# Performance work log

Hardware: AMD Instinct MI355X
Metric: run time of the kernel (lower is better)

## Reference

```python
import jax, jax.numpy as jnp
import numpy as np

N_NODES = 100000
N_EDGES = 1000000
DIM = 64


def rel_graph_conv(x, src, dst, etype, W, Ws, b, act):
    # DGL RelGraphConv (regularizer=None, self_loop=True, bias=True, sum agg):
    # out_i = act( sum_{(j->i)} W_{r} x_j + x_i @ Ws + b )
    # num_rels=2: transform once per relation, then select per edge.
    h = jnp.einsum('nd,rdo->rno', x, W)              # [2, N, out]
    m = jnp.where((etype == 0)[:, None], h[0][src], h[1][src])  # [E, out]
    agg = jax.ops.segment_sum(m, dst, num_segments=x.shape[0])  # [N, out]
    out = agg + x @ Ws + b
    return act(out) if act is not None else out


def setup_inputs() -> dict:
    key = jax.random.key(0)
    ks = jax.random.split(key, 16)
    scale = 1.0 / np.sqrt(DIM)
    inp = {
        'features': jax.random.normal(ks[0], (N_NODES, DIM), dtype=jnp.float32),
        'src': jax.random.randint(ks[1], (N_EDGES,), 0, N_NODES, dtype=jnp.int32),
        'dst': jax.random.randint(ks[2], (N_EDGES,), 0, N_NODES, dtype=jnp.int32),
        'etype': jax.random.randint(ks[3], (N_EDGES,), 0, 2, dtype=jnp.int32),
    }
    for i in range(3):
        inp[f'W{i}'] = jax.random.normal(ks[4 + 3 * i], (2, DIM, DIM), dtype=jnp.float32) * scale
        inp[f'Ws{i}'] = jax.random.normal(ks[5 + 3 * i], (DIM, DIM), dtype=jnp.float32) * scale
        inp[f'b{i}'] = jnp.zeros((DIM,), dtype=jnp.float32)
    return inp


def reference(features, src, dst, etype, W0, Ws0, b0, W1, Ws1, b1, W2, Ws2, b2):
    # dropout is identity in eval mode
    h = rel_graph_conv(features, src, dst, etype, W0, Ws0, b0, jax.nn.relu)
    h = rel_graph_conv(h, src, dst, etype, W1, Ws1, b1, jax.nn.relu)
    h = rel_graph_conv(h, src, dst, etype, W2, Ws2, b2, None)
    return h
```

## Files before the change

### kernel.cpp

```cpp
#include <hip/hip_runtime.h>

#define NN 100000
#define NE 1000000
#define NEP (NE + 6 * NN)
#define DIM 64
#define ZPITCH 200
#define SCHUNK 1024
#define SBLOCKS ((NN + SCHUNK - 1) / SCHUNK)
#define PAD4(c) (((c) + 3) & ~3)

typedef __attribute__((ext_vector_type(8))) short short8;
typedef __attribute__((ext_vector_type(4))) float f32x4;
typedef __attribute__((ext_vector_type(4))) _Float16 h4;
typedef __attribute__((ext_vector_type(8))) _Float16 h8;

union HU { uint2 u; h4 h; };

__device__ __forceinline__ ushort f2h(float f) {
    union { _Float16 h; ushort u; } c; c.h = (_Float16)f; return c.u;
}

__global__ __launch_bounds__(256) void zero_counts2(int* cnt2) {
    int i = blockIdx.x * 256 + threadIdx.x;
    if (i < 2 * NN) cnt2[i] = 0;
}

__global__ __launch_bounds__(256) void init_esrc(int* esrc) {
    int i = blockIdx.x * 256 + threadIdx.x;
    if (i < NEP) esrc[i] = NN;
}

__global__ __launch_bounds__(256) void count_rank2(const int* __restrict__ dst,
                                                   const int* __restrict__ et,
                                                   int* __restrict__ cnt2,
                                                   int* __restrict__ rank) {
    int e = blockIdx.x * 256 + threadIdx.x;
    if (e < NE) rank[e] = atomicAdd(&cnt2[dst[e] * 2 + et[e]], 1);
}

__global__ __launch_bounds__(256) void scan_partial2p(const int* __restrict__ cnt2,
                                                      int* __restrict__ bsum) {
    int t = threadIdx.x, lane = t & 63, wid = t >> 6;
    int base = blockIdx.x * SCHUNK + t * 4;
    int s = 0;
#pragma unroll
    for (int k = 0; k < 4; ++k) {
        int i = base + k;
        if (i < NN) s += PAD4(cnt2[2 * i]) + PAD4(cnt2[2 * i + 1]);
    }
#pragma unroll
    for (int off = 32; off > 0; off >>= 1) s += __shfl_down(s, off, 64);
    __shared__ int wtot[4];
    if (lane == 0) wtot[wid] = s;
    __syncthreads();
    if (t == 0) bsum[blockIdx.x] = wtot[0] + wtot[1] + wtot[2] + wtot[3];
}

__global__ __launch_bounds__(128) void scan_bsums(const int* __restrict__ bsum,
                                                  int* __restrict__ bsum_ex) {
    __shared__ int sh[128];
    int t = threadIdx.x;
    int v = (t < SBLOCKS) ? bsum[t] : 0;
    sh[t] = v;
    __syncthreads();
    for (int off = 1; off < 128; off <<= 1) {
        int u = (t >= off) ? sh[t - off] : 0;
        __syncthreads();
        sh[t] += u;
        __syncthreads();
    }
    if (t < SBLOCKS) bsum_ex[t] = sh[t] - v;
}

__global__ __launch_bounds__(256) void scan_final2p(const int* __restrict__ cnt2,
                                                    const int* __restrict__ bsum_ex,
                                                    int* __restrict__ row_ptr) {
    int t = threadIdx.x, lane = t & 63, wid = t >> 6;
    int base = blockIdx.x * SCHUNK + t * 4;
    int c[4];
#pragma unroll
    for (int k = 0; k < 4; ++k) {
        int i = base + k;
        c[k] = (i < NN) ? (PAD4(cnt2[2 * i]) + PAD4(cnt2[2 * i + 1])) : 0;
    }
    int s = c[0] + c[1] + c[2] + c[3];
    int incl = s;
#pragma unroll
    for (int off = 1; off < 64; off <<= 1) {
        int u = __shfl_up(incl, off, 64);
        if (lane >= off) incl += u;
    }
    __shared__ int wtot[4];
    if (lane == 63) wtot[wid] = incl;
    __syncthreads();
    int woff = 0;
    for (int w = 0; w < wid; ++w) woff += wtot[w];
    int run = bsum_ex[blockIdx.x] + woff + (incl - s);
#pragma unroll
    for (int k = 0; k < 4; ++k) {
        int i = base + k;
        if (i < NN) row_ptr[i] = run;
        run += c[k];
    }
}

__global__ __launch_bounds__(256) void fill_edges4(const int* __restrict__ src,
                                                   const int* __restrict__ dst,
                                                   const int* __restrict__ et,
                                                   const int* __restrict__ rank,
                                                   const int* __restrict__ row_ptr,
                                                   const int* __restrict__ cnt2,
                                                   int* __restrict__ esrc) {
    int e = blockIdx.x * 256 + threadIdx.x;
    if (e < NE) {
        int d = dst[e], r = et[e];
        int pos = row_ptr[d] + rank[e] + (r ? PAD4(cnt2[2 * d]) : 0);
        esrc[pos] = src[e];
    }
}

__global__ __launch_bounds__(256) void convert_feat(const float* __restrict__ x,
                                                    ushort* __restrict__ xb) {
    int i = blockIdx.x * 256 + threadIdx.x;
    float4 v = ((const float4*)x)[i];
    union { ushort u[4]; uint2 w; } o;
    o.u[0] = f2h(v.x); o.u[1] = f2h(v.y); o.u[2] = f2h(v.z); o.u[3] = f2h(v.w);
    *(uint2*)(xb + (size_t)i * 4) = o.w;
}

__global__ void zero_rows(ushort* a, ushort* b) {
    int t = threadIdx.x;
    a[(size_t)NN * DIM + t] = 0;
    b[(size_t)NN * DIM + t] = 0;
}

__global__ __launch_bounds__(256) void prep_w(const float* __restrict__ W,
                                              const float* __restrict__ Ws,
                                              ushort* __restrict__ wt) {
    int idx = blockIdx.x * 256 + threadIdx.x;
    int k = idx >> 6, n = idx & 63;
    float v = (k < 128) ? W[k * 64 + n] : Ws[(k - 128) * 64 + n];
    wt[n * 192 + k] = f2h(v);
}

__global__ __launch_bounds__(256) void rgcn_aggregate_q(
    const uint2* __restrict__ xb2, const int* __restrict__ row_ptr,
    const int* __restrict__ cnt2, const int* __restrict__ esrc,
    uint2* __restrict__ agg2)
{
    int t = threadIdx.x, lane = t & 63, wid = t >> 6;
    int n = blockIdx.x * 4 + wid;
    if (n >= NN) return;
    int g = lane >> 4, s = lane & 15;
    int start = row_ptr[n];
    int c0p = PAD4(cnt2[2 * n]);
    int c1p = PAD4(cnt2[2 * n + 1]);
    int degp = c0p + c1p;
    int g4 = g << 2;

    const uint2* xrow = xb2 + s;
    HU z; z.u.x = 0u; z.u.y = 0u;
    h4 a0 = z.h, a1 = z.h;

    for (int base = 0; base < degp; base += 64) {
        int rem = degp - base; if (rem > 64) rem = 64;
        int ev = (lane < rem) ? esrc[start + base + lane] : (int)NN;
        int b0 = c0p - base;
        if (b0 < 0) b0 = 0; if (b0 > rem) b0 = rem;
        int j = 0;
#pragma unroll 2
        for (; j < b0; j += 4) {
            int p = __builtin_amdgcn_ds_bpermute((j << 2) + g4, ev);
            HU v; v.u = xrow[(size_t)p * 16];
            a0 += v.h;
        }
#pragma unroll 2
        for (; j < rem; j += 4) {
            int p = __builtin_amdgcn_ds_bpermute((j << 2) + g4, ev);
            HU v; v.u = xrow[(size_t)p * 16];
            a1 += v.h;
        }
    }

    {
        HU x, r;
        x.h = a0;
        r.u.x = (uint)__shfl_xor((int)x.u.x, 16, 64);
        r.u.y = (uint)__shfl_xor((int)x.u.y, 16, 64);
        a0 = a0 + r.h;
        x.h = a0;
        r.u.x = (uint)__shfl_xor((int)x.u.x, 32, 64);
        r.u.y = (uint)__shfl_xor((int)x.u.y, 32, 64);
        a0 = a0 + r.h;
        x.h = a1;
        r.u.x = (uint)__shfl_xor((int)x.u.x, 16, 64);
        r.u.y = (uint)__shfl_xor((int)x.u.y, 16, 64);
        a1 = a1 + r.h;
        x.h = a1;
        r.u.x = (uint)__shfl_xor((int)x.u.x, 32, 64);
        r.u.y = (uint)__shfl_xor((int)x.u.y, 32, 64);
        a1 = a1 + r.h;
    }

    if (g < 2) {
        HU o; o.h = g ? a1 : a0;
        agg2[(size_t)n * 32 + g * 16 + s] = o.u;
    }
}

__global__ __launch_bounds__(256) void rgcn_transform_mfma(
    const ushort* __restrict__ agg,
    const ushort* __restrict__ xb,
    const ushort* __restrict__ wt,
    const float* __restrict__ bias,
    float* __restrict__ outf,
    ushort* __restrict__ xbn,
    int mode)
{
    __shared__ ushort sZ[64 * ZPITCH];

    int t = threadIdx.x, lane = t & 63, wid = t >> 6;
    int quad = lane >> 4, l16 = lane & 15;

    h8 bh[6];
    {
        const ushort* wh = wt + (size_t)(wid * 16 + l16) * 192;
#pragma unroll
        for (int kk = 0; kk < 6; ++kk)
            bh[kk] = *(const h8*)(wh + kk * 32 + quad * 8);
    }
    float bv = bias[wid * 16 + l16];

    int n0 = blockIdx.x * 64;
    for (int i = t; i < 1024; i += 256) {
        int node = i >> 4, c8 = i & 15;
        int n = n0 + node;
        uint4 v = {0u, 0u, 0u, 0u};
        if (n < NN) v = *(const uint4*)(agg + (size_t)n * 128 + c8 * 8);
        *(uint4*)(sZ + node * ZPITCH + c8 * 8) = v;
    }
    for (int i = t; i < 512; i += 256) {
        int node = i >> 3, c8 = i & 7;
        int n = n0 + node;
        uint4 v = {0u, 0u, 0u, 0u};
        if (n < NN) v = *(const uint4*)(xb + (size_t)n * DIM + c8 * 8);
        *(uint4*)(sZ + node * ZPITCH + 128 + c8 * 8) = v;
    }
    __syncthreads();

    f32x4 acc[4];
#pragma unroll
    for (int mt = 0; mt < 4; ++mt) acc[mt] = (f32x4){bv, bv, bv, bv};

#pragma unroll
    for (int kk = 0; kk < 6; ++kk) {
#pragma unroll
        for (int mt = 0; mt < 4; ++mt) {
            h8 a = *(const h8*)(sZ + (mt * 16 + l16) * ZPITCH + kk * 32 + quad * 8);
            acc[mt] = __builtin_amdgcn_mfma_f32_16x16x32_f16(a, bh[kk], acc[mt], 0, 0, 0);
        }
    }

    int col = wid * 16 + l16;
#pragma unroll
    for (int mt = 0; mt < 4; ++mt) {
#pragma unroll
        for (int r = 0; r < 4; ++r) {
            int node = n0 + mt * 16 + quad * 4 + r;
            if (node < NN) {
                float v = acc[mt][r];
                if (mode) outf[(size_t)node * DIM + col] = v;
                else      xbn[(size_t)node * DIM + col] = f2h(fmaxf(v, 0.f));
            }
        }
    }
}

extern "C" void kernel_launch(void* const* d_in, const int* in_sizes, int n_in,
                              void* d_out, int out_size, void* d_ws, size_t ws_size,
                              hipStream_t stream)
{
    const float* feat = (const float*)d_in[0];
    const int*   src  = (const int*)d_in[1];
    const int*   dst  = (const int*)d_in[2];
    const int*   et   = (const int*)d_in[3];
    const float* W[3]  = { (const float*)d_in[4], (const float*)d_in[7], (const float*)d_in[10] };
    const float* Ws[3] = { (const float*)d_in[5], (const float*)d_in[8], (const float*)d_in[11] };
    const float* b[3]  = { (const float*)d_in[6], (const float*)d_in[9], (const float*)d_in[12] };

    uint*   agg   = (uint*)d_ws;
    ushort* xbuf0 = (ushort*)(agg + (size_t)NN * 64);
    ushort* xbuf1 = xbuf0 + (size_t)(NN + 1) * DIM;
    ushort* wt    = xbuf1 + (size_t)(NN + 1) * DIM;
    int* esrc    = (int*)(wt + 3 * 12288);
    int* rank    = esrc + NEP;
    int* cnt2    = rank + NE;
    int* row_ptr = cnt2 + 2 * NN;
    int* bsum    = row_ptr + NN;
    int* bsum_ex = bsum + SBLOCKS;
    float* outF  = (float*)d_out;

    const dim3 tb(256);
    const int zgrid = (2 * NN + 255) / 256;
    const int igrid = (NEP + 255) / 256;
    const int egrid = (NE + 255) / 256;
    const int tgrid = (NN + 63) / 64;
    const int agrid = NN / 4;

    zero_counts2<<<zgrid, tb, 0, stream>>>(cnt2);
    init_esrc<<<igrid, tb, 0, stream>>>(esrc);
    count_rank2<<<egrid, tb, 0, stream>>>(dst, et, cnt2, rank);
    scan_partial2p<<<SBLOCKS, tb, 0, stream>>>(cnt2, bsum);
    scan_bsums<<<1, 128, 0, stream>>>(bsum, bsum_ex);
    scan_final2p<<<SBLOCKS, tb, 0, stream>>>(cnt2, bsum_ex, row_ptr);
    fill_edges4<<<egrid, tb, 0, stream>>>(src, dst, et, rank, row_ptr, cnt2, esrc);

    prep_w<<<48, tb, 0, stream>>>(W[0], Ws[0], wt);
    prep_w<<<48, tb, 0, stream>>>(W[1], Ws[1], wt + 12288);
    prep_w<<<48, tb, 0, stream>>>(W[2], Ws[2], wt + 2 * 12288);
    convert_feat<<<NN * 16 / 256, tb, 0, stream>>>(feat, xbuf0);
    zero_rows<<<1, 64, 0, stream>>>(xbuf0, xbuf1);

    rgcn_aggregate_q<<<agrid, tb, 0, stream>>>((const uint2*)xbuf0, row_ptr, cnt2, esrc, (uint2*)agg);
    rgcn_transform_mfma<<<tgrid, tb, 0, stream>>>((const ushort*)agg, xbuf0, wt, b[0], nullptr, xbuf1, 0);
    rgcn_aggregate_q<<<agrid, tb, 0, stream>>>((const uint2*)xbuf1, row_ptr, cnt2, esrc, (uint2*)agg);
    rgcn_transform_mfma<<<tgrid, tb, 0, stream>>>((const ushort*)agg, xbuf1, wt + 12288, b[1], nullptr, xbuf0, 0);
    rgcn_aggregate_q<<<agrid, tb, 0, stream>>>((const uint2*)xbuf0, row_ptr, cnt2, esrc, (uint2*)agg);
    rgcn_transform_mfma<<<tgrid, tb, 0, stream>>>((const ushort*)agg, xbuf0, wt + 2 * 12288, b[2], outF, nullptr, 1);
}
```

Baseline: 345.5 us.

## Partition degree counting atomics and map one node per 16-lane group in aggregation

Edge counting now uses eight privatized count arrays chosen by block index, followed by a merge kernel that produces per-partition prefix offsets used when filling the CSR. This spreads atomic contention across more addresses. The aggregation kernel now assigns one destination node per 16-lane group instead of one per wavefront, loading four edge indices with a vector load rather than using bpermute shuffles and cross-group reductions. The cost is more zeroing work, an extra kernel, and more divergence between groups with different degrees inside a wave.

```diff
diff --git a/kernel.cpp b/kernel.cpp
--- a/kernel.cpp
+++ b/kernel.cpp
@@ -8,6 +8,7 @@
 #define SCHUNK 1024
 #define SBLOCKS ((NN + SCHUNK - 1) / SCHUNK)
 #define PAD4(c) (((c) + 3) & ~3)
+#define NPART 8
 
 typedef __attribute__((ext_vector_type(8))) short short8;
 typedef __attribute__((ext_vector_type(4))) float f32x4;
@@ -20,9 +21,9 @@
     union { _Float16 h; ushort u; } c; c.h = (_Float16)f; return c.u;
 }
 
-__global__ __launch_bounds__(256) void zero_counts2(int* cnt2) {
+__global__ __launch_bounds__(256) void zero_buf(int* p, int len) {
     int i = blockIdx.x * 256 + threadIdx.x;
-    if (i < 2 * NN) cnt2[i] = 0;
+    if (i < len) p[i] = 0;
 }
 
 __global__ __launch_bounds__(256) void init_esrc(int* esrc) {
@@ -30,12 +31,28 @@
     if (i < NEP) esrc[i] = NN;
 }
 
-__global__ __launch_bounds__(256) void count_rank2(const int* __restrict__ dst,
-                                                   const int* __restrict__ et,
-                                                   int* __restrict__ cnt2,
-                                                   int* __restrict__ rank) {
+__global__ __launch_bounds__(256) void count_rank2p(const int* __restrict__ dst,
+                                                    const int* __restrict__ et,
+                                                    int* __restrict__ cnt2p,
+                                                    int* __restrict__ rank) {
     int e = blockIdx.x * 256 + threadIdx.x;
-    if (e < NE) rank[e] = atomicAdd(&cnt2[dst[e] * 2 + et[e]], 1);
+    int p = blockIdx.x & (NPART - 1);
+    if (e < NE) rank[e] = atomicAdd(&cnt2p[p * 2 * NN + dst[e] * 2 + et[e]], 1);
+}
+
+__global__ __launch_bounds__(256) void merge_counts(int* __restrict__ cnt2p,
+                                                    int* __restrict__ cnt2) {
+    int i = blockIdx.x * 256 + threadIdx.x;
+    if (i < 2 * NN) {
+        int s = 0;
+#pragma unroll
+        for (int p = 0; p < NPART; ++p) {
+            int v = cnt2p[p * 2 * NN + i];
+            cnt2p[p * 2 * NN + i] = s;
+            s += v;
+        }
+        cnt2[i] = s;
+    }
 }
 
 __global__ __launch_bounds__(256) void scan_partial2p(const int* __restrict__ cnt2,
@@ -104,17 +121,20 @@
     }
 }
 
-__global__ __launch_bounds__(256) void fill_edges4(const int* __restrict__ src,
-                                                   const int* __restrict__ dst,
-                                                   const int* __restrict__ et,
-                                                   const int* __restrict__ rank,
-                                                   const int* __restrict__ row_ptr,
-                                                   const int* __restrict__ cnt2,
-                                                   int* __restrict__ esrc) {
+__global__ __launch_bounds__(256) void fill_edges4p(const int* __restrict__ src,
+                                                    const int* __restrict__ dst,
+                                                    const int* __restrict__ et,
+                                                    const int* __restrict__ rank,
+                                                    const int* __restrict__ row_ptr,
+                                                    const int* __restrict__ cnt2,
+                                                    const int* __restrict__ cnt2p,
+                                                    int* __restrict__ esrc) {
     int e = blockIdx.x * 256 + threadIdx.x;
+    int p = blockIdx.x & (NPART - 1);
     if (e < NE) {
         int d = dst[e], r = et[e];
-        int pos = row_ptr[d] + rank[e] + (r ? PAD4(cnt2[2 * d]) : 0);
+        int pre = cnt2p[p * 2 * NN + 2 * d + r];
+        int pos = row_ptr[d] + pre + rank[e] + (r ? PAD4(cnt2[2 * d]) : 0);
         esrc[pos] = src[e];
     }
 }
@@ -143,69 +163,47 @@
     wt[n * 192 + k] = f2h(v);
 }
 
-__global__ __launch_bounds__(256) void rgcn_aggregate_q(
+__global__ __launch_bounds__(256) void rgcn_aggregate_g(
     const uint2* __restrict__ xb2, const int* __restrict__ row_ptr,
     const int* __restrict__ cnt2, const int* __restrict__ esrc,
     uint2* __restrict__ agg2)
 {
     int t = threadIdx.x, lane = t & 63, wid = t >> 6;
-    int n = blockIdx.x * 4 + wid;
-    if (n >= NN) return;
     int g = lane >> 4, s = lane & 15;
+    int n = blockIdx.x * 16 + wid * 4 + g;
     int start = row_ptr[n];
     int c0p = PAD4(cnt2[2 * n]);
-    int c1p = PAD4(cnt2[2 * n + 1]);
-    int degp = c0p + c1p;
-    int g4 = g << 2;
+    int degp = c0p + PAD4(cnt2[2 * n + 1]);
 
     const uint2* xrow = xb2 + s;
     HU z; z.u.x = 0u; z.u.y = 0u;
     h4 a0 = z.h, a1 = z.h;
 
-    for (int base = 0; base < degp; base += 64) {
-        int rem = degp - base; if (rem > 64) rem = 64;
-        int ev = (lane < rem) ? esrc[start + base + lane] : (int)NN;
-        int b0 = c0p - base;
-        if (b0 < 0) b0 = 0; if (b0 > rem) b0 = rem;
-        int j = 0;
+    int j = 0;
 #pragma unroll 2
-        for (; j < b0; j += 4) {
-            int p = __builtin_amdgcn_ds_bpermute((j << 2) + g4, ev);
-            HU v; v.u = xrow[(size_t)p * 16];
-            a0 += v.h;
-        }
+    for (; j < c0p; j += 4) {
+        int4 q = *(const int4*)(esrc + start + j);
+        HU v0, v1, v2, v3;
+        v0.u = xrow[(size_t)q.x * 16];
+        v1.u = xrow[(size_t)q.y * 16];
+        v2.u = xrow[(size_t)q.z * 16];
+        v3.u = xrow[(size_t)q.w * 16];
+        a0 += v0.h; a0 += v1.h; a0 += v2.h; a0 += v3.h;
+    }
 #pragma unroll 2
-        for (; j < rem; j += 4) {
-            int p = __builtin_amdgcn_ds_bpermute((j << 2) + g4, ev);
-            HU v; v.u = xrow[(size_t)p * 16];
-            a1 += v.h;
-        }
-    }
-
-    {
-        HU x, r;
-        x.h = a0;
-        r.u.x = (uint)__shfl_xor((int)x.u.x, 16, 64);
-        r.u.y = (uint)__shfl_xor((int)x.u.y, 16, 64);
-        a0 = a0 + r.h;
-        x.h = a0;
-        r.u.x = (uint)__shfl_xor((int)x.u.x, 32, 64);
-        r.u.y = (uint)__shfl_xor((int)x.u.y, 32, 64);
-        a0 = a0 + r.h;
-        x.h = a1;
-        r.u.x = (uint)__shfl_xor((int)x.u.x, 16, 64);
-        r.u.y = (uint)__shfl_xor((int)x.u.y, 16, 64);
-        a1 = a1 + r.h;
-        x.h = a1;
-        r.u.x = (uint)__shfl_xor((int)x.u.x, 32, 64);
-        r.u.y = (uint)__shfl_xor((int)x.u.y, 32, 64);
-        a1 = a1 + r.h;
-    }
-
-    if (g < 2) {
-        HU o; o.h = g ? a1 : a0;
-        agg2[(size_t)n * 32 + g * 16 + s] = o.u;
-    }
+    for (; j < degp; j += 4) {
+        int4 q = *(const int4*)(esrc + start + j);
+        HU v0, v1, v2, v3;
+        v0.u = xrow[(size_t)q.x * 16];
+        v1.u = xrow[(size_t)q.y * 16];
+        v2.u = xrow[(size_t)q.z * 16];
+        v3.u = xrow[(size_t)q.w * 16];
+        a1 += v0.h; a1 += v1.h; a1 += v2.h; a1 += v3.h;
+    }
+
+    HU o0, o1; o0.h = a0; o1.h = a1;
+    agg2[(size_t)n * 32 + s] = o0.u;
+    agg2[(size_t)n * 32 + 16 + s] = o1.u;
 }
 
 __global__ __launch_bounds__(256) void rgcn_transform_mfma(
@@ -295,25 +293,28 @@
     int* esrc    = (int*)(wt + 3 * 12288);
     int* rank    = esrc + NEP;
     int* cnt2    = rank + NE;
-    int* row_ptr = cnt2 + 2 * NN;
+    int* cnt2p   = cnt2 + 2 * NN;
+    int* row_ptr = cnt2p + NPART * 2 * NN;
     int* bsum    = row_ptr + NN;
     int* bsum_ex = bsum + SBLOCKS;
     float* outF  = (float*)d_out;
 
     const dim3 tb(256);
-    const int zgrid = (2 * NN + 255) / 256;
+    const int zgrid = (NPART * 2 * NN + 255) / 256;
     const int igrid = (NEP + 255) / 256;
     const int egrid = (NE + 255) / 256;
+    const int mgrid = (2 * NN + 255) / 256;
     const int tgrid = (NN + 63) / 64;
-    const int agrid = NN / 4;
-
-    zero_counts2<<<zgrid, tb, 0, stream>>>(cnt2);
+    const int agrid = NN / 16;
+
+    zero_buf<<<zgrid, tb, 0, stream>>>(cnt2p, NPART * 2 * NN);
     init_esrc<<<igrid, tb, 0, stream>>>(esrc);
-    count_rank2<<<egrid, tb, 0, stream>>>(dst, et, cnt2, rank);
+    count_rank2p<<<egrid, tb, 0, stream>>>(dst, et, cnt2p, rank);
+    merge_counts<<<mgrid, tb, 0, stream>>>(cnt2p, cnt2);
     scan_partial2p<<<SBLOCKS, tb, 0, stream>>>(cnt2, bsum);
     scan_bsums<<<1, 128, 0, stream>>>(bsum, bsum_ex);
     scan_final2p<<<SBLOCKS, tb, 0, stream>>>(cnt2, bsum_ex, row_ptr);
-    fill_edges4<<<egrid, tb, 0, stream>>>(src, dst, et, rank, row_ptr, cnt2, esrc);
+    fill_edges4p<<<egrid, tb, 0, stream>>>(src, dst, et, rank, row_ptr, cnt2, cnt2p, esrc);
 
     prep_w<<<48, tb, 0, stream>>>(W[0], Ws[0], wt);
     prep_w<<<48, tb, 0, stream>>>(W[1], Ws[1], wt + 12288);
@@ -321,10 +322,10 @@
     convert_feat<<<NN * 16 / 256, tb, 0, stream>>>(feat, xbuf0);
     zero_rows<<<1, 64, 0, stream>>>(xbuf0, xbuf1);
 
-    rgcn_aggregate_q<<<agrid, tb, 0, stream>>>((const uint2*)xbuf0, row_ptr, cnt2, esrc, (uint2*)agg);
+    rgcn_aggregate_g<<<agrid, tb, 0, stream>>>((const uint2*)xbuf0, row_ptr, cnt2, esrc, (uint2*)agg);
     rgcn_transform_mfma<<<tgrid, tb, 0, stream>>>((const ushort*)agg, xbuf0, wt, b[0], nullptr, xbuf1, 0);
-    rgcn_aggregate_q<<<agrid, tb, 0, stream>>>((const uint2*)xbuf1, row_ptr, cnt2, esrc, (uint2*)agg);
+    rgcn_aggregate_g<<<agrid, tb, 0, stream>>>((const uint2*)xbuf1, row_ptr, cnt2, esrc, (uint2*)agg);
     rgcn_transform_mfma<<<tgrid, tb, 0, stream>>>((const ushort*)agg, xbuf1, wt + 12288, b[1], nullptr, xbuf0, 0);
-    rgcn_aggregate_q<<<agrid, tb, 0, stream>>>((const uint2*)xbuf0, row_ptr, cnt2, esrc, (uint2*)agg);
+    rgcn_aggregate_g<<<agrid, tb, 0, stream>>>((const uint2*)xbuf0, row_ptr, cnt2, esrc, (uint2*)agg);
     rgcn_transform_mfma<<<tgrid, tb, 0, stream>>>((const ushort*)agg, xbuf0, wt + 2 * 12288, b[2], outF, nullptr, 1);
 }
```

Result: faster. 313.2 us (-9.4%).
